# Performance work log

Measured on AMD Instinct MI355X. Metric: run time of the kernel, lower is better.

## Reference

```python
import jax, jax.numpy as jnp
import numpy as np
from jax import lax

E = 1024      # embed_dim
H = 16        # num_heads
HD = E // H   # head_dim = 64
GS = 2        # head_group_size
G = H // GS   # num head groups = 8
KQ = 3        # kq kernel q size
KK = 3        # kq kernel k size


def setup_inputs() -> dict:
    key = jax.random.key(0)
    ks = jax.random.split(key, 18)
    B, S = 2, 1024
    def rn(k, shape, scale=1.0):
        return jax.random.normal(k, shape, dtype=jnp.float32) * scale
    return {
        "Q": rn(ks[0], (B, S, E)),
        "K": rn(ks[1], (B, S, E)),
        "V": rn(ks[2], (B, S, E)),
        "Wq": rn(ks[3], (E, E), 0.02), "bq": rn(ks[4], (E,), 0.02),
        "Wk": rn(ks[5], (E, E), 0.02), "bk": rn(ks[6], (E,), 0.02),
        "Wv": rn(ks[7], (E, E), 0.02), "bv": rn(ks[8], (E,), 0.02),
        "Wo": rn(ks[9], (E, E), 0.02), "bo": rn(ks[10], (E,), 0.02),
        # depthwise key-query conv: [out=H, in/groups=1, KQ, KK]
        "kq_w": rn(ks[11], (H, 1, KQ, KK), 0.1),
        "kq_b": rn(ks[12], (H,), 0.02),
        # grouped 1x1 head-mix conv: weight [H, GS] (kernel dim squeezed), bias [H]
        "mix_w": rn(ks[13], (H, GS), 0.3),
        "mix_b": rn(ks[14], (H,), 0.02),
        # DynamicTanh params over head_dim (channels_last)
        "dyt_alpha": jnp.array([0.5], dtype=jnp.float32),
        "dyt_w": jnp.ones((HD,), dtype=jnp.float32),
        "dyt_b": jnp.zeros((HD,), dtype=jnp.float32),
        "depth_scale": jnp.ones((1,), dtype=jnp.float32),
    }


def reference(Q, K, V, Wq, bq, Wk, bk, Wv, bv, Wo, bo,
              kq_w, kq_b, mix_w, mix_b, dyt_alpha, dyt_w, dyt_b, depth_scale):
    B, S, _ = Q.shape
    scale = HD ** (-0.5)
    # projections -> [B, H, S, HD]
    q = (Q @ Wq + bq).reshape(B, S, H, HD).transpose(0, 2, 1, 3)
    k = (K @ Wk + bk).reshape(B, S, H, HD).transpose(0, 2, 1, 3)
    v = (V @ Wv + bv).reshape(B, S, H, HD).transpose(0, 2, 1, 3)

    # raw logits [B, H, Sq, Sk], multiplicative causal mask (zeros above diag)
    logits = jnp.einsum('bhqd,bhkd->bhqk', q, k) * scale
    causal = jnp.tril(jnp.ones((S, S), dtype=logits.dtype))
    logits = logits * causal

    # per-head (depthwise) key-query conv2d; torch pads q-dim by 2 both sides
    # then crops to first S rows (causal in q), k-dim padded symmetrically by 1
    conv = lax.conv_general_dilated(
        logits, kq_w, window_strides=(1, 1),
        padding=[(KQ - 1, KQ - 1), ((KK - 1) // 2, (KK - 1) // 2)],
        dimension_numbers=('NCHW', 'OIHW', 'NCHW'),
        feature_group_count=H)
    conv = conv + kq_b[None, :, None, None]
    conv = conv[:, :, :S, :]

    attn = jax.nn.softmax(conv, axis=-1)

    # grouped 1x1 head-mixing conv (within groups of GS heads) + bias
    attn_g = attn.reshape(B, G, GS, S, S)
    mw = mix_w.reshape(G, GS, GS)  # [group, out_in_group, in_in_group]
    mixed = jnp.einsum('goj,bgjqk->bgoqk', mw, attn_g).reshape(B, H, S, S)
    mixed = mixed + mix_b[None, :, None, None]

    out = jnp.einsum('bhqk,bhkd->bhqd', mixed, v)
    # DynamicTanh over head_dim (channels_last) + depth scale
    out = jnp.tanh(dyt_alpha * out) * dyt_w + dyt_b
    out = out * depth_scale
    out = out.transpose(0, 2, 1, 3).reshape(B, S, E)
    return out @ Wo + bo
```

## Files before the change

kernel.cpp:

```cpp
#include <hip/hip_runtime.h>
#include <cstdint>
#include <cstddef>

typedef __bf16 bf16;
typedef __bf16 bf16x8 __attribute__((ext_vector_type(8)));
typedef float f32x4 __attribute__((ext_vector_type(4)));

#define DEVI static __device__ __forceinline__

DEVI unsigned int cvt_pk_bf16(float lo, float hi) {
  unsigned int bl = __float_as_uint(lo);
  bl += 0x7fffu + ((bl >> 16) & 1u);
  unsigned int bh = __float_as_uint(hi);
  bh += 0x7fffu + ((bh >> 16) & 1u);
  return (bl >> 16) | (bh & 0xffff0000u);
}
DEVI float bf_lo(unsigned int u) { return __uint_as_float(u << 16); }
DEVI float bf_hi(unsigned int u) { return __uint_as_float(u & 0xffff0000u); }

__global__ __launch_bounds__(256) void wtr_k(
    const float* __restrict__ Wq, const float* __restrict__ Wk,
    const float* __restrict__ Wv, const float* __restrict__ Wo,
    bf16* __restrict__ Wt)
{
  const int z = blockIdx.z;
  const float* W = (z == 0) ? Wq : (z == 1) ? Wk : (z == 2) ? Wv : Wo;
  bf16* out = Wt + ((size_t)z << 20);
  const int n0 = blockIdx.x * 64, k0 = blockIdx.y * 64;
  __shared__ bf16 Ts[64 * 72];
  const int tid = threadIdx.x;
  #pragma unroll
  for (int i = 0; i < 4; ++i) {
    int t = tid + i * 256;
    int kr = t >> 4, nc = t & 15;
    float4 v = *(const float4*)(W + (size_t)(k0 + kr) * 1024 + n0 + nc * 4);
    Ts[(nc * 4 + 0) * 72 + kr] = (bf16)v.x;
    Ts[(nc * 4 + 1) * 72 + kr] = (bf16)v.y;
    Ts[(nc * 4 + 2) * 72 + kr] = (bf16)v.z;
    Ts[(nc * 4 + 3) * 72 + kr] = (bf16)v.w;
  }
  __syncthreads();
  const int n = tid >> 2, kc = tid & 3;
  *(uint4*)(out + (size_t)(n0 + n) * 1024 + k0 + kc * 16) =
      *(const uint4*)(&Ts[n * 72 + kc * 16]);
  *(uint4*)(out + (size_t)(n0 + n) * 1024 + k0 + kc * 16 + 8) =
      *(const uint4*)(&Ts[n * 72 + kc * 16 + 8]);
}

__global__ __launch_bounds__(256) void proj_gemm_k(
    const float* __restrict__ Q, const float* __restrict__ K,
    const float* __restrict__ V, const bf16* __restrict__ Wt,
    const float* __restrict__ bq, const float* __restrict__ bk,
    const float* __restrict__ bv, bf16* __restrict__ outbase)
{
  const int z = blockIdx.z;
  const float* A = (z == 0) ? Q : (z == 1) ? K : V;
  const bf16* Bt = Wt + ((size_t)z << 20);
  const float* bias = (z == 0) ? bq : (z == 1) ? bk : bv;
  bf16* outb = outbase + ((size_t)z << 21);

  __shared__ __align__(16) char sm[10240];
  bf16* As = (bf16*)sm;
  bf16* Bs = As + 64 * 40;
  bf16* T2 = (bf16*)sm;

  const int tid = threadIdx.x, lane = tid & 63, wid = tid >> 6;
  const int q4 = lane >> 4, n16 = lane & 15;
  const int wm = wid >> 1, wn = wid & 1;
  const int bid = blockIdx.x;
  const int m0 = (bid & 31) * 64, n0 = (bid >> 5) * 64;
  const int brow = tid >> 2, bc = tid & 3;
  f32x4 acc[2][2] = {};

  float4 aR0 = *(const float4*)(A + (size_t)(m0 + brow) * 1024 + bc * 8);
  float4 aR1 = *(const float4*)(A + (size_t)(m0 + brow) * 1024 + bc * 8 + 4);
  uint4 bR = *(const uint4*)(Bt + (size_t)(n0 + brow) * 1024 + bc * 8);
  for (int kb = 0; kb < 32; ++kb) {
    __syncthreads();
    *(uint2*)(&As[brow * 40 + bc * 8]) =
        make_uint2(cvt_pk_bf16(aR0.x, aR0.y), cvt_pk_bf16(aR0.z, aR0.w));
    *(uint2*)(&As[brow * 40 + bc * 8 + 4]) =
        make_uint2(cvt_pk_bf16(aR1.x, aR1.y), cvt_pk_bf16(aR1.z, aR1.w));
    *(uint4*)(&Bs[brow * 40 + bc * 8]) = bR;
    __syncthreads();
    if (kb < 31) {
      const int k1 = (kb + 1) * 32;
      aR0 = *(const float4*)(A + (size_t)(m0 + brow) * 1024 + k1 + bc * 8);
      aR1 = *(const float4*)(A + (size_t)(m0 + brow) * 1024 + k1 + bc * 8 + 4);
      bR  = *(const uint4*)(Bt + (size_t)(n0 + brow) * 1024 + k1 + bc * 8);
    }
    bf16x8 af[2], bfv[2];
    #pragma unroll
    for (int rt = 0; rt < 2; ++rt)
      af[rt] = *(const bf16x8*)(&As[(wm * 32 + rt * 16 + n16) * 40 + q4 * 8]);
    #pragma unroll
    for (int ct = 0; ct < 2; ++ct)
      bfv[ct] = *(const bf16x8*)(&Bs[(wn * 32 + ct * 16 + n16) * 40 + q4 * 8]);
    #pragma unroll
    for (int rt = 0; rt < 2; ++rt)
      #pragma unroll
      for (int ct = 0; ct < 2; ++ct)
        acc[rt][ct] = __builtin_amdgcn_mfma_f32_16x16x32_bf16(af[rt], bfv[ct], acc[rt][ct], 0, 0, 0);
  }

  if (z < 2) {
    #pragma unroll
    for (int ct = 0; ct < 2; ++ct) {
      int col = n0 + wn * 32 + ct * 16 + n16;
      float bvl = bias[col];
      int h = col >> 6, d = col & 63;
      #pragma unroll
      for (int rt = 0; rt < 2; ++rt) {
        #pragma unroll
        for (int r = 0; r < 4; ++r) {
          int row = m0 + wm * 32 + rt * 16 + q4 * 4 + r;
          int b2 = row >> 10, s = row & 1023;
          outb[((size_t)((b2 * 16 + h) * 1024 + s) << 6) + d] =
              (bf16)(acc[rt][ct][r] + bvl);
        }
      }
    }
  } else {
    __syncthreads();
    #pragma unroll
    for (int ct = 0; ct < 2; ++ct) {
      int cl = wn * 32 + ct * 16 + n16;
      float bvl = bias[n0 + cl];
      #pragma unroll
      for (int rt = 0; rt < 2; ++rt)
        #pragma unroll
        for (int r = 0; r < 4; ++r) {
          int rl = wm * 32 + rt * 16 + q4 * 4 + r;
          T2[cl * 72 + rl] = (bf16)(acc[rt][ct][r] + bvl);
        }
    }
    __syncthreads();
    const int b2 = m0 >> 10, kt = (m0 & 1023) >> 6, h = n0 >> 6;
    bf16* vout = outb + ((size_t)(b2 * 16 + h) << 16) + kt * 4096;
    #pragma unroll
    for (int i = 0; i < 2; ++i) {
      int c = tid + i * 256;
      int kk = c >> 8, ctt = (c >> 6) & 3, q4c = (c >> 4) & 3, n16c = c & 15;
      uint4 v = *(const uint4*)(&T2[(ctt * 16 + n16c) * 72 + kk * 32 + q4c * 8]);
      *(uint4*)(vout + kk * 2048 + ctt * 512 + (q4c * 16 + n16c) * 8) = v;
    }
  }
}

__global__ __launch_bounds__(256) void out_gemm_k(
    const bf16* __restrict__ Ab, const bf16* __restrict__ Bt,
    const float* __restrict__ bias, float* __restrict__ outf)
{
  __shared__ __align__(16) char sm[10240];
  bf16* As = (bf16*)sm;
  bf16* Bs = As + 64 * 40;
  const int tid = threadIdx.x, lane = tid & 63, wid = tid >> 6;
  const int q4 = lane >> 4, n16 = lane & 15;
  const int wm = wid >> 1, wn = wid & 1;
  const int bid = blockIdx.x;
  const int m0 = (bid & 31) * 64, n0 = (bid >> 5) * 64;
  const int brow = tid >> 2, bc = tid & 3;
  f32x4 acc[2][2] = {};

  uint4 aR = *(const uint4*)(Ab + (size_t)(m0 + brow) * 1024 + bc * 8);
  uint4 bR = *(const uint4*)(Bt + (size_t)(n0 + brow) * 1024 + bc * 8);
  for (int kb = 0; kb < 32; ++kb) {
    __syncthreads();
    *(uint4*)(&As[brow * 40 + bc * 8]) = aR;
    *(uint4*)(&Bs[brow * 40 + bc * 8]) = bR;
    __syncthreads();
    if (kb < 31) {
      const int k1 = (kb + 1) * 32;
      aR = *(const uint4*)(Ab + (size_t)(m0 + brow) * 1024 + k1 + bc * 8);
      bR = *(const uint4*)(Bt + (size_t)(n0 + brow) * 1024 + k1 + bc * 8);
    }
    bf16x8 af[2], bfv[2];
    #pragma unroll
    for (int rt = 0; rt < 2; ++rt)
      af[rt] = *(const bf16x8*)(&As[(wm * 32 + rt * 16 + n16) * 40 + q4 * 8]);
    #pragma unroll
    for (int ct = 0; ct < 2; ++ct)
      bfv[ct] = *(const bf16x8*)(&Bs[(wn * 32 + ct * 16 + n16) * 40 + q4 * 8]);
    #pragma unroll
    for (int rt = 0; rt < 2; ++rt)
      #pragma unroll
      for (int ct = 0; ct < 2; ++ct)
        acc[rt][ct] = __builtin_amdgcn_mfma_f32_16x16x32_bf16(af[rt], bfv[ct], acc[rt][ct], 0, 0, 0);
  }
  #pragma unroll
  for (int ct = 0; ct < 2; ++ct) {
    int col = n0 + wn * 32 + ct * 16 + n16;
    float bvl = bias[col];
    #pragma unroll
    for (int rt = 0; rt < 2; ++rt)
      #pragma unroll
      for (int r = 0; r < 4; ++r) {
        int row = m0 + wm * 32 + rt * 16 + q4 * 4 + r;
        outf[(size_t)row * 1024 + col] = acc[rt][ct][r] + bvl;
      }
  }
}

__global__ void vtile_sum_k(const bf16* __restrict__ V2, float* __restrict__ Tsum)
{
  int kt = blockIdx.x, h = blockIdx.y, b = blockIdx.z, d = threadIdx.x;
  int ctt = d >> 4, n16c = d & 15;
  const bf16* p = V2 + ((size_t)(b * 16 + h) << 16) + kt * 4096 + ctt * 512 + n16c * 8;
  float s = 0.f;
  #pragma unroll
  for (int kk = 0; kk < 2; ++kk)
    #pragma unroll
    for (int q4i = 0; q4i < 4; ++q4i)
      #pragma unroll
      for (int j = 0; j < 8; ++j)
        s += (float)p[kk * 2048 + q4i * 128 + j];
  Tsum[((b * 16 + h) * 16 + kt) * 64 + d] = s;
}

__global__ void vtail_k(const float* __restrict__ Tsum, float* __restrict__ Vtail)
{
  int h = blockIdx.x, b = blockIdx.y, d = threadIdx.x;
  float c = 0.f;
  Vtail[((b * 16 + h) * 17 + 16) * 64 + d] = 0.f;
  for (int kt = 15; kt >= 0; --kt) {
    c += Tsum[((b * 16 + h) * 16 + kt) * 64 + d];
    Vtail[((b * 16 + h) * 17 + kt) * 64 + d] = c;
  }
}

__global__ __launch_bounds__(320) void logits_conv_k(
    const bf16* __restrict__ qh, const bf16* __restrict__ kh,
    const float* __restrict__ kq_w, const float* __restrict__ kq_b,
    bf16* __restrict__ conv_out, float* __restrict__ tstats)
{
  const int tt = blockIdx.x;
  int qt = 0, base = 0;
  while (qt < 15 && base + qt + 2 <= tt) { base += qt + 2; ++qt; }
  const int ct = tt - base;
  const int h = blockIdx.y, b = blockIdx.z;
  const int q0 = qt * 64, c0 = ct * 64;
  __shared__ __align__(16) char un[18432];
  bf16* Kst = (bf16*)un;
  float* Ls = (float*)un;
  const int tid = threadIdx.x;
  const int lane = tid & 63, wid = tid >> 6;
  const int q4 = lane >> 4, n16 = lane & 15;
  const bf16* qb = qh + ((size_t)(b * 16 + h) << 16);
  const bf16* kb = kh + ((size_t)(b * 16 + h) << 16);

  const int ar = min(max(q0 - 2 + wid * 16 + n16, 0), 1023);
  bf16x8 a0 = *(const bf16x8*)(qb + ar * 64 + q4 * 8);
  bf16x8 a1 = *(const bf16x8*)(qb + ar * 64 + 32 + q4 * 8);

  for (int t = tid; t < 640; t += 320) {
    int row = t >> 3, ch = t & 7;
    int br = min(max(c0 - 1 + row, 0), 1023);
    *(uint4*)(&Kst[row * 72 + ch * 8]) = *(const uint4*)(kb + br * 64 + ch * 8);
  }
  __syncthreads();

  f32x4 acc[5] = {};
  #pragma unroll
  for (int c5 = 0; c5 < 5; ++c5) {
    int brow = c5 * 16 + n16;
    bf16x8 b0 = *(const bf16x8*)(&Kst[brow * 72 + q4 * 8]);
    bf16x8 b1 = *(const bf16x8*)(&Kst[brow * 72 + 32 + q4 * 8]);
    acc[c5] = __builtin_amdgcn_mfma_f32_16x16x32_bf16(a0, b0, acc[c5], 0, 0, 0);
    acc[c5] = __builtin_amdgcn_mfma_f32_16x16x32_bf16(a1, b1, acc[c5], 0, 0, 0);
  }
  __syncthreads();

  #pragma unroll
  for (int c5 = 0; c5 < 5; ++c5) {
    #pragma unroll
    for (int r = 0; r < 4; ++r) {
      int Lrow = wid * 16 + q4 * 4 + r;
      int Lcol = c5 * 16 + n16;
      if (Lrow < 66 && Lcol < 66) {
        int rg = q0 - 2 + Lrow;
        int cg = c0 - 1 + Lcol;
        float v = (cg >= 0 && cg <= rg) ? acc[c5][r] * 0.125f : 0.f;
        Ls[Lrow * 68 + Lcol] = v;
      }
    }
  }
  __syncthreads();

  if (tid < 256) {
    float w9[9];
    #pragma unroll
    for (int i = 0; i < 9; ++i) w9[i] = kq_w[h * 9 + i];
    const float bb = kq_b[h];
    const size_t tplane = (size_t)(b * 16 + h) * 151 + base + ct;
    bf16* tb = conv_out + tplane * 4096;
    float2* st = (float2*)tstats + tplane * 64;

    const int r = tid >> 2, qr = tid & 3;
    float4 R0[5], R1[5], R2[5];
    const float* L0 = &Ls[r * 68 + qr * 16];
    #pragma unroll
    for (int i = 0; i < 5; ++i) {
      R0[i] = *(const float4*)(L0 + i * 4);
      R1[i] = *(const float4*)(L0 + 68 + i * 4);
      R2[i] = *(const float4*)(L0 + 136 + i * 4);
    }
    const float* f0 = (const float*)R0;
    const float* f1 = (const float*)R1;
    const float* f2 = (const float*)R2;
    float o[16];
    #pragma unroll
    for (int jj = 0; jj < 16; ++jj)
      o[jj] = bb + w9[0]*f0[jj] + w9[1]*f0[jj+1] + w9[2]*f0[jj+2]
                 + w9[3]*f1[jj] + w9[4]*f1[jj+1] + w9[5]*f1[jj+2]
                 + w9[6]*f2[jj] + w9[7]*f2[jj+1] + w9[8]*f2[jj+2];
    float mx = o[0];
    #pragma unroll
    for (int jj = 1; jj < 16; ++jj) mx = fmaxf(mx, o[jj]);
    mx = fmaxf(mx, __shfl_xor(mx, 1));
    mx = fmaxf(mx, __shfl_xor(mx, 2));
    unsigned int p[8];
    #pragma unroll
    for (int jj = 0; jj < 8; ++jj)
      p[jj] = cvt_pk_bf16(__expf(o[2*jj] - mx), __expf(o[2*jj+1] - mx));
    const int kk = qr >> 1, q4b = (qr & 1) * 2, sr = r >> 4, n16r = r & 15;
    *(uint4*)(tb + (sr * 2 + kk) * 512 + (q4b * 16 + n16r) * 8)       = *(const uint4*)&p[0];
    *(uint4*)(tb + (sr * 2 + kk) * 512 + ((q4b + 1) * 16 + n16r) * 8) = *(const uint4*)&p[4];
    float s = 0.f;
    #pragma unroll
    for (int jj = 0; jj < 8; ++jj) s += bf_lo(p[jj]) + bf_hi(p[jj]);
    s += __shfl_xor(s, 1);
    s += __shfl_xor(s, 2);
    if (qr == 0) st[r] = make_float2(mx, s);
  }
}

__global__ __launch_bounds__(256) void combine_k(
    const float* __restrict__ tstats, const float* __restrict__ kq_b,
    float* __restrict__ rs)
{
  const int ridx = blockIdx.x * 256 + threadIdx.x;
  const int q = ridx & 1023, h = (ridx >> 10) & 15, plane = ridx >> 10;
  const int qt = q >> 6;
  const int nkt = min(qt + 2, 16);
  const int Tc = 1024 - (nkt << 6);
  const float2* ts = (const float2*)tstats +
      ((size_t)plane * 151 + (size_t)(qt * (qt + 3) / 2)) * 64 + (q & 63);
  const float kb = kq_b[h];
  float mx = (Tc > 0) ? kb : -3.0e38f;
  for (int kt = 0; kt < nkt; ++kt) mx = fmaxf(mx, ts[(size_t)kt * 64].x);
  float s = (float)Tc * __expf(kb - mx);
  for (int kt = 0; kt < nkt; ++kt) {
    float2 v = ts[(size_t)kt * 64];
    s += v.y * __expf(v.x - mx);
  }
  rs[(size_t)ridx * 2]     = mx;
  rs[(size_t)ridx * 2 + 1] = 1.f / s;
}

__global__ __launch_bounds__(256) void pv_k(
    const bf16* __restrict__ conv_out, const bf16* __restrict__ V2,
    const float* __restrict__ rs, const float* __restrict__ tstats,
    const float* __restrict__ Vtail,
    const float* __restrict__ mix_w, const float* __restrict__ mix_b,
    const float* __restrict__ kq_b,
    const float* __restrict__ dyt_alpha, const float* __restrict__ dyt_w,
    const float* __restrict__ dyt_b, const float* __restrict__ depth_scale,
    bf16* __restrict__ out_attn)
{
  const int qt16 = blockIdx.x, g = blockIdx.y, b = blockIdx.z;
  const int qt = qt16 >> 2;
  const int nkt = min(qt + 2, 16);
  const int Tc = 1024 - (nkt << 6);
  const int tid = threadIdx.x, lane = tid & 63, wid = tid >> 6;
  const int q4 = lane >> 4, n16 = lane & 15;
  const int oo = wid >> 1, kh = wid & 1;
  const int h0 = 2 * g, ho = h0 + oo;
  const int sr = qt16 & 3, strow = sr * 16;
  const size_t tbase = (size_t)(qt * (qt + 3) / 2);

  const int qrow = qt16 * 16 + n16;
  const float2 r0 = *(const float2*)(rs + ((((size_t)(b * 16 + h0)     << 10) + qrow) << 1));
  const float2 r1 = *(const float2*)(rs + ((((size_t)(b * 16 + h0 + 1) << 10) + qrow) << 1));
  const float m0 = r0.x, m1 = r1.x;
  const float mwa = mix_w[ho * 2 + 0], mwb = mix_w[ho * 2 + 1];
  const float wa = mwa * r0.y, wb = mwb * r1.y;

  const bf16* pb0 = conv_out +
      ((size_t)(b * 16 + h0) * 151 + tbase) * 4096 + sr * 1024 + lane * 8;
  const bf16* pb1 = pb0 + (size_t)151 * 4096;
  const float2* ts0 = (const float2*)tstats +
      ((size_t)(b * 16 + h0) * 151 + tbase) * 64 + strow + n16;
  const float2* ts1 = ts0 + (size_t)151 * 64;
  const bf16* vb = V2 + ((size_t)(b * 16 + ho) << 16) + lane * 8;

  const int niter = (nkt - kh + 1) >> 1;
  float wk0[8], wk1[8];
  #pragma unroll
  for (int i = 0; i < 8; ++i) {
    int ktc = (i < niter) ? (kh + 2 * i) : 0;
    wk0[i] = wa * __expf(ts0[(size_t)ktc * 64].x - m0);
    wk1[i] = wb * __expf(ts1[(size_t)ktc * 64].x - m1);
  }

  f32x4 acc[4] = {};
  int ii = 0;
  for (int kt = kh; kt < nkt; kt += 2, ++ii) {
    uint4 u0[2], u1[2];
    #pragma unroll
    for (int kk = 0; kk < 2; ++kk) {
      u0[kk] = *(const uint4*)(pb0 + (size_t)kt * 4096 + kk * 512);
      u1[kk] = *(const uint4*)(pb1 + (size_t)kt * 4096 + kk * 512);
    }
    bf16x8 bv[2][4];
    #pragma unroll
    for (int kk = 0; kk < 2; ++kk)
      #pragma unroll
      for (int ctt = 0; ctt < 4; ++ctt)
        bv[kk][ctt] = *(const bf16x8*)(vb + (size_t)kt * 4096 + kk * 2048 + ctt * 512);
    const float w0 = wk0[ii], w1 = wk1[ii];
    #pragma unroll
    for (int kk = 0; kk < 2; ++kk) {
      bf16x8 af;
      const unsigned int* a0p = (const unsigned int*)&u0[kk];
      const unsigned int* a1p = (const unsigned int*)&u1[kk];
      #pragma unroll
      for (int i2 = 0; i2 < 4; ++i2) {
        float a0 = w0 * bf_lo(a0p[i2]) + w1 * bf_lo(a1p[i2]);
        float a1 = w0 * bf_hi(a0p[i2]) + w1 * bf_hi(a1p[i2]);
        ((unsigned int*)&af)[i2] = cvt_pk_bf16(a0, a1);
      }
      #pragma unroll
      for (int ctt = 0; ctt < 4; ++ctt)
        acc[ctt] = __builtin_amdgcn_mfma_f32_16x16x32_bf16(af, bv[kk][ctt], acc[ctt], 0, 0, 0);
    }
  }

  __shared__ float Pp[2][16][64];
  if (kh == 1) {
    #pragma unroll
    for (int ctt = 0; ctt < 4; ++ctt)
      #pragma unroll
      for (int r = 0; r < 4; ++r)
        Pp[oo][q4 * 4 + r][ctt * 16 + n16] = acc[ctt][r];
  }
  __syncthreads();
  if (kh == 1) return;
  #pragma unroll
  for (int ctt = 0; ctt < 4; ++ctt)
    #pragma unroll
    for (int r = 0; r < 4; ++r)
      acc[ctt][r] += Pp[oo][q4 * 4 + r][ctt * 16 + n16];

  const float kqb0 = kq_b[h0], kqb1 = kq_b[h0 + 1];
  float tw[4];
  #pragma unroll
  for (int r = 0; r < 4; ++r) {
    int qr = qt16 * 16 + q4 * 4 + r;
    float2 s0 = *(const float2*)(rs + ((((size_t)(b * 16 + h0)     << 10) + qr) << 1));
    float2 s1 = *(const float2*)(rs + ((((size_t)(b * 16 + h0 + 1) << 10) + qr) << 1));
    tw[r] = (Tc > 0) ? (mwa * s0.y * __expf(kqb0 - s0.x) +
                        mwb * s1.y * __expf(kqb1 - s1.x)) : 0.f;
  }
  const float mb = mix_b[ho];
  const float alpha = dyt_alpha[0], dsc = depth_scale[0];
  const float* vt = Vtail + (size_t)(b * 16 + ho) * 17 * 64;
  #pragma unroll
  for (int ctt = 0; ctt < 4; ++ctt) {
    int d = ctt * 16 + n16;
    float vtn = vt[(size_t)nkt * 64 + d];
    float vt0 = vt[d];
    float wgt = dyt_w[d], bds = dyt_b[d];
    #pragma unroll
    for (int r = 0; r < 4; ++r) {
      float v = acc[ctt][r] + tw[r] * vtn + mb * vt0;
      float e = __expf(2.f * alpha * v);
      float th = 1.f - 2.f / (e + 1.f);
      float y = (th * wgt + bds) * dsc;
      int qr = qt16 * 16 + q4 * 4 + r;
      out_attn[(((size_t)(b * 1024 + qr)) << 10) + ho * 64 + d] = (bf16)y;
    }
  }
}

extern "C" void kernel_launch(void* const* d_in, const int* in_sizes, int n_in,
                              void* d_out, int out_size, void* d_ws, size_t ws_size,
                              hipStream_t stream) {
  const float* Q    = (const float*)d_in[0];
  const float* Kx   = (const float*)d_in[1];
  const float* V    = (const float*)d_in[2];
  const float* Wq   = (const float*)d_in[3];
  const float* bq   = (const float*)d_in[4];
  const float* Wk   = (const float*)d_in[5];
  const float* bk   = (const float*)d_in[6];
  const float* Wv   = (const float*)d_in[7];
  const float* bv   = (const float*)d_in[8];
  const float* Wo   = (const float*)d_in[9];
  const float* bo   = (const float*)d_in[10];
  const float* kq_w = (const float*)d_in[11];
  const float* kq_b = (const float*)d_in[12];
  const float* mixw = (const float*)d_in[13];
  const float* mixb = (const float*)d_in[14];
  const float* dyta = (const float*)d_in[15];
  const float* dytw = (const float*)d_in[16];
  const float* dytb = (const float*)d_in[17];
  const float* dsc  = (const float*)d_in[18];

  char* ws = (char*)d_ws;
  bf16* qh     = (bf16*)(ws);
  float* tstat = (float*)(ws + (size_t)(12 << 20));
  float* Vtail = (float*)(ws + (size_t)(16 << 20));
  float* Tsum  = (float*)(ws + (size_t)(16 << 20) + (256 << 10));
  float* rsbuf = (float*)(ws + (size_t)(16 << 20) + (512 << 10));
  bf16* WtT    = (bf16*)(ws + (size_t)(17 << 20));
  bf16* oat    = (bf16*)(ws + (size_t)(17 << 20));
  bf16* conv   = (bf16*)(ws + (size_t)(25 << 20));
  bf16* kh     = qh + ((size_t)1 << 21);
  bf16* V2     = qh + ((size_t)2 << 21);

  wtr_k<<<dim3(16, 16, 4), 256, 0, stream>>>(Wq, Wk, Wv, Wo, WtT);
  proj_gemm_k<<<dim3(512, 1, 3), 256, 0, stream>>>(Q, Kx, V, WtT, bq, bk, bv, qh);
  vtile_sum_k<<<dim3(16, 16, 2), 64, 0, stream>>>(V2, Tsum);
  vtail_k<<<dim3(16, 2), 64, 0, stream>>>(Tsum, Vtail);
  logits_conv_k<<<dim3(151, 16, 2), 320, 0, stream>>>(qh, kh, kq_w, kq_b, conv, tstat);
  combine_k<<<dim3(128), 256, 0, stream>>>(tstat, kq_b, rsbuf);
  pv_k<<<dim3(64, 8, 2), 256, 0, stream>>>(conv, V2, rsbuf, tstat, Vtail, mixw, mixb, kq_b,
                                           dyta, dytw, dytb, dsc, oat);
  out_gemm_k<<<dim3(512), 256, 0, stream>>>(oat, WtT + ((size_t)3 << 20), bo, (float*)d_out);
}
```

Before: 220.8 us.

## Pre-convert inputs to bf16 and use async global-to-LDS double-buffered GEMMs

Adds a kernel that converts Q/K/V from fp32 to bf16 up front. The projection and output GEMMs now load tiles with global_load_lds straight into XOR-swizzled, double-buffered LDS, and the projection tile grows to 128x64. The V epilogue writes packed results directly instead of staging a transpose through LDS. This removes register-staged loads and one barrier per k-step, at the cost of an extra conversion pass and extra workspace traffic.

New measurement: 218.6 us. About the same (-1.0%).

```diff
diff --git a/kernel.cpp b/kernel.cpp
--- a/kernel.cpp
+++ b/kernel.cpp
@@ -17,6 +17,12 @@
 }
 DEVI float bf_lo(unsigned int u) { return __uint_as_float(u << 16); }
 DEVI float bf_hi(unsigned int u) { return __uint_as_float(u & 0xffff0000u); }
+
+DEVI void gload16(const bf16* g, bf16* l) {
+  __builtin_amdgcn_global_load_lds(
+      (const __attribute__((address_space(1))) unsigned int*)g,
+      (__attribute__((address_space(3))) unsigned int*)l, 16, 0, 0);
+}
 
 __global__ __launch_bounds__(256) void wtr_k(
     const float* __restrict__ Wq, const float* __restrict__ Wk,
@@ -47,145 +53,165 @@
       *(const uint4*)(&Ts[n * 72 + kc * 16 + 8]);
 }
 
+__global__ __launch_bounds__(256) void a2bf_k(
+    const float* __restrict__ Q, const float* __restrict__ K,
+    const float* __restrict__ V, bf16* __restrict__ Ab)
+{
+  const int z = blockIdx.y;
+  const float* A = (z == 0) ? Q : (z == 1) ? K : V;
+  bf16* o = Ab + ((size_t)z << 21);
+  const int idx = blockIdx.x * 256 + threadIdx.x;
+  const float4 v0 = *(const float4*)(A + (size_t)idx * 8);
+  const float4 v1 = *(const float4*)(A + (size_t)idx * 8 + 4);
+  uint4 u;
+  u.x = cvt_pk_bf16(v0.x, v0.y);
+  u.y = cvt_pk_bf16(v0.z, v0.w);
+  u.z = cvt_pk_bf16(v1.x, v1.y);
+  u.w = cvt_pk_bf16(v1.z, v1.w);
+  *(uint4*)(o + (size_t)idx * 8) = u;
+}
+
 __global__ __launch_bounds__(256) void proj_gemm_k(
-    const float* __restrict__ Q, const float* __restrict__ K,
-    const float* __restrict__ V, const bf16* __restrict__ Wt,
+    const bf16* __restrict__ Ab, const bf16* __restrict__ Wt,
     const float* __restrict__ bq, const float* __restrict__ bk,
     const float* __restrict__ bv, bf16* __restrict__ outbase)
 {
   const int z = blockIdx.z;
-  const float* A = (z == 0) ? Q : (z == 1) ? K : V;
+  const bf16* A  = Ab + ((size_t)z << 21);
   const bf16* Bt = Wt + ((size_t)z << 20);
   const float* bias = (z == 0) ? bq : (z == 1) ? bk : bv;
   bf16* outb = outbase + ((size_t)z << 21);
 
-  __shared__ __align__(16) char sm[10240];
-  bf16* As = (bf16*)sm;
-  bf16* Bs = As + 64 * 40;
-  bf16* T2 = (bf16*)sm;
-
+  __shared__ __align__(16) bf16 As[2][4096];
+  __shared__ __align__(16) bf16 Bs[2][2048];
+
+  const int tid = threadIdx.x, lane = tid & 63, wid = tid >> 6;
+  const int q4 = lane >> 4, n16 = lane & 15;
+  const int wm = wid >> 1, wn = wid & 1;
+  const int bid = blockIdx.x;
+  const int m0 = (bid & 15) * 128, n0 = (bid >> 4) * 64;
+
+  const int cA0 = wid * 64 + lane, cA1 = cA0 + 256;
+  const bf16* gA0 = A + (size_t)(m0 + (cA0 >> 2)) * 1024 + (((cA0 & 3) ^ ((cA0 >> 3) & 3)) << 3);
+  const bf16* gA1 = A + (size_t)(m0 + (cA1 >> 2)) * 1024 + (((cA1 & 3) ^ ((cA1 >> 3) & 3)) << 3);
+  const bf16* gB  = Bt + (size_t)(n0 + (cA0 >> 2)) * 1024 + (((cA0 & 3) ^ ((cA0 >> 3) & 3)) << 3);
+  const int qsw = (q4 ^ ((n16 >> 1) & 3)) << 4;
+
+  f32x4 acc[4][2] = {};
+
+  gload16(gA0, &As[0][wid * 512]);
+  gload16(gA1, &As[0][2048 + wid * 512]);
+  gload16(gB,  &Bs[0][wid * 512]);
+  __syncthreads();
+
+  int cur = 0;
+  for (int kb = 0; kb < 32; ++kb) {
+    if (kb < 31) {
+      const int kc = (kb + 1) * 32;
+      gload16(gA0 + kc, &As[cur ^ 1][wid * 512]);
+      gload16(gA1 + kc, &As[cur ^ 1][2048 + wid * 512]);
+      gload16(gB + kc,  &Bs[cur ^ 1][wid * 512]);
+    }
+    const char* ab = (const char*)&As[cur][0];
+    const char* bb = (const char*)&Bs[cur][0];
+    bf16x8 af[4], bfv[2];
+    #pragma unroll
+    for (int rt = 0; rt < 4; ++rt)
+      af[rt] = *(const bf16x8*)(ab + (wm * 64 + rt * 16 + n16) * 64 + qsw);
+    #pragma unroll
+    for (int ct = 0; ct < 2; ++ct)
+      bfv[ct] = *(const bf16x8*)(bb + (wn * 32 + ct * 16 + n16) * 64 + qsw);
+    #pragma unroll
+    for (int rt = 0; rt < 4; ++rt)
+      #pragma unroll
+      for (int ct = 0; ct < 2; ++ct)
+        acc[rt][ct] = __builtin_amdgcn_mfma_f32_16x16x32_bf16(af[rt], bfv[ct], acc[rt][ct], 0, 0, 0);
+    __syncthreads();
+    cur ^= 1;
+  }
+
+  if (z < 2) {
+    const int h = n0 >> 6;
+    #pragma unroll
+    for (int ct = 0; ct < 2; ++ct) {
+      const int dl = wn * 32 + ct * 16 + n16;
+      const float bvl = bias[n0 + dl];
+      #pragma unroll
+      for (int rt = 0; rt < 4; ++rt) {
+        #pragma unroll
+        for (int r = 0; r < 4; ++r) {
+          int row = m0 + wm * 64 + rt * 16 + q4 * 4 + r;
+          int b2 = row >> 10, s = row & 1023;
+          outb[((size_t)((b2 * 16 + h) * 1024 + s) << 6) + dl] =
+              (bf16)(acc[rt][ct][r] + bvl);
+        }
+      }
+    }
+  } else {
+    const int b2 = m0 >> 10, kt0 = (m0 & 1023) >> 6, hh = n0 >> 6;
+    bf16* vout = outb + ((size_t)(b2 * 16 + hh) << 16) + (size_t)(kt0 + wm) * 4096;
+    #pragma unroll
+    for (int rt = 0; rt < 4; ++rt) {
+      const int kk = rt >> 1;
+      const int q4c = (rt & 1) * 2 + (q4 >> 1);
+      const int jo = (q4 & 1) * 4;
+      #pragma unroll
+      for (int ct = 0; ct < 2; ++ct) {
+        const int cl = wn * 32 + ct * 16 + n16;
+        const float bvl = bias[n0 + cl];
+        unsigned int p0 = cvt_pk_bf16(acc[rt][ct][0] + bvl, acc[rt][ct][1] + bvl);
+        unsigned int p1 = cvt_pk_bf16(acc[rt][ct][2] + bvl, acc[rt][ct][3] + bvl);
+        *(uint2*)(vout + kk * 2048 + (wn * 2 + ct) * 512 + (q4c * 16 + n16) * 8 + jo) =
+            make_uint2(p0, p1);
+      }
+    }
+  }
+}
+
+__global__ __launch_bounds__(256) void out_gemm_k(
+    const bf16* __restrict__ Ab, const bf16* __restrict__ Bt,
+    const float* __restrict__ bias, float* __restrict__ outf)
+{
+  __shared__ __align__(16) bf16 As[2][2048];
+  __shared__ __align__(16) bf16 Bs[2][2048];
   const int tid = threadIdx.x, lane = tid & 63, wid = tid >> 6;
   const int q4 = lane >> 4, n16 = lane & 15;
   const int wm = wid >> 1, wn = wid & 1;
   const int bid = blockIdx.x;
   const int m0 = (bid & 31) * 64, n0 = (bid >> 5) * 64;
-  const int brow = tid >> 2, bc = tid & 3;
+  const int c = wid * 64 + lane;
+  const bf16* gA = Ab + (size_t)(m0 + (c >> 2)) * 1024 + (((c & 3) ^ ((c >> 3) & 3)) << 3);
+  const bf16* gB = Bt + (size_t)(n0 + (c >> 2)) * 1024 + (((c & 3) ^ ((c >> 3) & 3)) << 3);
+  const int qsw = (q4 ^ ((n16 >> 1) & 3)) << 4;
   f32x4 acc[2][2] = {};
 
-  float4 aR0 = *(const float4*)(A + (size_t)(m0 + brow) * 1024 + bc * 8);
-  float4 aR1 = *(const float4*)(A + (size_t)(m0 + brow) * 1024 + bc * 8 + 4);
-  uint4 bR = *(const uint4*)(Bt + (size_t)(n0 + brow) * 1024 + bc * 8);
+  gload16(gA, &As[0][wid * 512]);
+  gload16(gB, &Bs[0][wid * 512]);
+  __syncthreads();
+
+  int cur = 0;
   for (int kb = 0; kb < 32; ++kb) {
-    __syncthreads();
-    *(uint2*)(&As[brow * 40 + bc * 8]) =
-        make_uint2(cvt_pk_bf16(aR0.x, aR0.y), cvt_pk_bf16(aR0.z, aR0.w));
-    *(uint2*)(&As[brow * 40 + bc * 8 + 4]) =
-        make_uint2(cvt_pk_bf16(aR1.x, aR1.y), cvt_pk_bf16(aR1.z, aR1.w));
-    *(uint4*)(&Bs[brow * 40 + bc * 8]) = bR;
-    __syncthreads();
     if (kb < 31) {
-      const int k1 = (kb + 1) * 32;
-      aR0 = *(const float4*)(A + (size_t)(m0 + brow) * 1024 + k1 + bc * 8);
-      aR1 = *(const float4*)(A + (size_t)(m0 + brow) * 1024 + k1 + bc * 8 + 4);
-      bR  = *(const uint4*)(Bt + (size_t)(n0 + brow) * 1024 + k1 + bc * 8);
-    }
+      const int kc = (kb + 1) * 32;
+      gload16(gA + kc, &As[cur ^ 1][wid * 512]);
+      gload16(gB + kc, &Bs[cur ^ 1][wid * 512]);
+    }
+    const char* ab = (const char*)&As[cur][0];
+    const char* bb = (const char*)&Bs[cur][0];
     bf16x8 af[2], bfv[2];
     #pragma unroll
     for (int rt = 0; rt < 2; ++rt)
-      af[rt] = *(const bf16x8*)(&As[(wm * 32 + rt * 16 + n16) * 40 + q4 * 8]);
+      af[rt] = *(const bf16x8*)(ab + (wm * 32 + rt * 16 + n16) * 64 + qsw);
     #pragma unroll
     for (int ct = 0; ct < 2; ++ct)
-      bfv[ct] = *(const bf16x8*)(&Bs[(wn * 32 + ct * 16 + n16) * 40 + q4 * 8]);
+      bfv[ct] = *(const bf16x8*)(bb + (wn * 32 + ct * 16 + n16) * 64 + qsw);
     #pragma unroll
     for (int rt = 0; rt < 2; ++rt)
       #pragma unroll
       for (int ct = 0; ct < 2; ++ct)
         acc[rt][ct] = __builtin_amdgcn_mfma_f32_16x16x32_bf16(af[rt], bfv[ct], acc[rt][ct], 0, 0, 0);
-  }
-
-  if (z < 2) {
-    #pragma unroll
-    for (int ct = 0; ct < 2; ++ct) {
-      int col = n0 + wn * 32 + ct * 16 + n16;
-      float bvl = bias[col];
-      int h = col >> 6, d = col & 63;
-      #pragma unroll
-      for (int rt = 0; rt < 2; ++rt) {
-        #pragma unroll
-        for (int r = 0; r < 4; ++r) {
-          int row = m0 + wm * 32 + rt * 16 + q4 * 4 + r;
-          int b2 = row >> 10, s = row & 1023;
-          outb[((size_t)((b2 * 16 + h) * 1024 + s) << 6) + d] =
-              (bf16)(acc[rt][ct][r] + bvl);
-        }
-      }
-    }
-  } else {
     __syncthreads();
-    #pragma unroll
-    for (int ct = 0; ct < 2; ++ct) {
-      int cl = wn * 32 + ct * 16 + n16;
-      float bvl = bias[n0 + cl];
-      #pragma unroll
-      for (int rt = 0; rt < 2; ++rt)
-        #pragma unroll
-        for (int r = 0; r < 4; ++r) {
-          int rl = wm * 32 + rt * 16 + q4 * 4 + r;
-          T2[cl * 72 + rl] = (bf16)(acc[rt][ct][r] + bvl);
-        }
-    }
-    __syncthreads();
-    const int b2 = m0 >> 10, kt = (m0 & 1023) >> 6, h = n0 >> 6;
-    bf16* vout = outb + ((size_t)(b2 * 16 + h) << 16) + kt * 4096;
-    #pragma unroll
-    for (int i = 0; i < 2; ++i) {
-      int c = tid + i * 256;
-      int kk = c >> 8, ctt = (c >> 6) & 3, q4c = (c >> 4) & 3, n16c = c & 15;
-      uint4 v = *(const uint4*)(&T2[(ctt * 16 + n16c) * 72 + kk * 32 + q4c * 8]);
-      *(uint4*)(vout + kk * 2048 + ctt * 512 + (q4c * 16 + n16c) * 8) = v;
-    }
-  }
-}
-
-__global__ __launch_bounds__(256) void out_gemm_k(
-    const bf16* __restrict__ Ab, const bf16* __restrict__ Bt,
-    const float* __restrict__ bias, float* __restrict__ outf)
-{
-  __shared__ __align__(16) char sm[10240];
-  bf16* As = (bf16*)sm;
-  bf16* Bs = As + 64 * 40;
-  const int tid = threadIdx.x, lane = tid & 63, wid = tid >> 6;
-  const int q4 = lane >> 4, n16 = lane & 15;
-  const int wm = wid >> 1, wn = wid & 1;
-  const int bid = blockIdx.x;
-  const int m0 = (bid & 31) * 64, n0 = (bid >> 5) * 64;
-  const int brow = tid >> 2, bc = tid & 3;
-  f32x4 acc[2][2] = {};
-
-  uint4 aR = *(const uint4*)(Ab + (size_t)(m0 + brow) * 1024 + bc * 8);
-  uint4 bR = *(const uint4*)(Bt + (size_t)(n0 + brow) * 1024 + bc * 8);
-  for (int kb = 0; kb < 32; ++kb) {
-    __syncthreads();
-    *(uint4*)(&As[brow * 40 + bc * 8]) = aR;
-    *(uint4*)(&Bs[brow * 40 + bc * 8]) = bR;
-    __syncthreads();
-    if (kb < 31) {
-      const int k1 = (kb + 1) * 32;
-      aR = *(const uint4*)(Ab + (size_t)(m0 + brow) * 1024 + k1 + bc * 8);
-      bR = *(const uint4*)(Bt + (size_t)(n0 + brow) * 1024 + k1 + bc * 8);
-    }
-    bf16x8 af[2], bfv[2];
-    #pragma unroll
-    for (int rt = 0; rt < 2; ++rt)
-      af[rt] = *(const bf16x8*)(&As[(wm * 32 + rt * 16 + n16) * 40 + q4 * 8]);
-    #pragma unroll
-    for (int ct = 0; ct < 2; ++ct)
-      bfv[ct] = *(const bf16x8*)(&Bs[(wn * 32 + ct * 16 + n16) * 40 + q4 * 8]);
-    #pragma unroll
-    for (int rt = 0; rt < 2; ++rt)
-      #pragma unroll
-      for (int ct = 0; ct < 2; ++ct)
-        acc[rt][ct] = __builtin_amdgcn_mfma_f32_16x16x32_bf16(af[rt], bfv[ct], acc[rt][ct], 0, 0, 0);
+    cur ^= 1;
   }
   #pragma unroll
   for (int ct = 0; ct < 2; ++ct) {
@@ -514,11 +540,13 @@
   bf16* WtT    = (bf16*)(ws + (size_t)(17 << 20));
   bf16* oat    = (bf16*)(ws + (size_t)(17 << 20));
   bf16* conv   = (bf16*)(ws + (size_t)(25 << 20));
+  bf16* Ab     = (bf16*)(ws + (size_t)(25 << 20));
   bf16* kh     = qh + ((size_t)1 << 21);
   bf16* V2     = qh + ((size_t)2 << 21);
 
   wtr_k<<<dim3(16, 16, 4), 256, 0, stream>>>(Wq, Wk, Wv, Wo, WtT);
-  proj_gemm_k<<<dim3(512, 1, 3), 256, 0, stream>>>(Q, Kx, V, WtT, bq, bk, bv, qh);
+  a2bf_k<<<dim3(1024, 3), 256, 0, stream>>>(Q, Kx, V, Ab);
+  proj_gemm_k<<<dim3(256, 1, 3), 256, 0, stream>>>(Ab, WtT, bq, bk, bv, qh);
   vtile_sum_k<<<dim3(16, 16, 2), 64, 0, stream>>>(V2, Tsum);
   vtail_k<<<dim3(16, 2), 64, 0, stream>>>(Tsum, Vtail);
   logits_conv_k<<<dim3(151, 16, 2), 320, 0, stream>>>(qh, kh, kq_w, kq_b, conv, tstat);
```
